# Optimization experiments

Measured on AMD Instinct MI355X. Metric: run time of the kernel, lower is better.

Reference implementation:

```python
import jax, jax.numpy as jnp
import numpy as np
import math

EPS = 1e-6  # PCEN eps


def _logit(p):
    return math.log(p / (1.0 - p))


def _pcen(mel, log_s, log_alpha, log_delta, log_r, dmin, dmax):
    """PCEN: per-channel energy normalization. mel: (B, M, T); params: (M,)."""
    s = jnp.clip(jax.nn.sigmoid(log_s), 0.05, 0.3)            # (M,)
    alpha = jnp.clip(jax.nn.sigmoid(log_alpha), 0.9, 0.999)   # (M,)
    delta = jnp.clip(jnp.exp(log_delta), dmin, dmax)          # (M,)
    r = jnp.clip(jax.nn.sigmoid(log_r), 0.05, 0.25)           # (M,)

    # IIR smoother over time: smoother_0 = mel[..., 0];
    # for t in 0..T-1: smoother = (1-s)*smoother + s*mel_t  (t=0 included -> smoothed_0 = mel_0)
    mel_t = jnp.transpose(mel, (2, 0, 1))  # (T, B, M)

    def step(sm, x):
        sm = (1.0 - s) * sm + s * x
        return sm, sm

    _, smoothed_t = jax.lax.scan(step, mel_t[0], mel_t)
    smoothed = jnp.transpose(smoothed_t, (1, 2, 0))  # (B, M, T)

    gain = (EPS + smoothed) ** (-alpha[None, :, None])
    d = delta[None, :, None]
    rr = r[None, :, None]
    return (mel * gain + d) ** rr - d ** rr


def setup_inputs() -> dict:
    key = jax.random.key(0)
    B, M, T = 64, 80, 4000
    mel = jax.random.uniform(key, (B, M, T), dtype=jnp.float32)
    f = jnp.full
    return {
        "mel": mel,
        # non-stationary expert PCEN (s=0.025, alpha=0.99, delta=2.0, r=0.5)
        "log_s_ns": f((M,), _logit(0.025), jnp.float32),
        "log_alpha_ns": f((M,), _logit(0.99), jnp.float32),
        "log_delta_ns": f((M,), math.log(2.0), jnp.float32),
        "log_r_ns": f((M,), _logit(0.5), jnp.float32),
        # stationary expert PCEN (s=0.15, alpha=0.99, delta=0.01, r=0.1)
        "log_s_st": f((M,), _logit(0.15), jnp.float32),
        "log_alpha_st": f((M,), _logit(0.99), jnp.float32),
        "log_delta_st": f((M,), math.log(0.01), jnp.float32),
        "log_r_st": f((M,), _logit(0.1), jnp.float32),
        "gate_temp": jnp.asarray(5.0, jnp.float32),
    }


def reference(mel, log_s_ns, log_alpha_ns, log_delta_ns, log_r_ns,
              log_s_st, log_alpha_st, log_delta_st, log_r_st, gate_temp):
    out_ns = _pcen(mel, log_s_ns, log_alpha_ns, log_delta_ns, log_r_ns, 0.5, 5.0)
    out_st = _pcen(mel, log_s_st, log_alpha_st, log_delta_st, log_r_st, 0.001, 0.1)

    # routing signal: spectral flatness + spectral tilt (0 learnable params)
    log_mel = jnp.log(mel + 1e-8)
    geo = jnp.exp(jnp.mean(log_mel, axis=1, keepdims=True))          # (B,1,T)
    arith = jnp.mean(mel, axis=1, keepdims=True) + 1e-8
    sf = jnp.clip(geo / arith, 0.0, 1.0)

    M = mel.shape[1]
    low = jnp.mean(mel[:, : M // 3, :], axis=1, keepdims=True)
    high = jnp.mean(mel[:, 2 * M // 3 :, :], axis=1, keepdims=True)
    tilt = jnp.clip(low / (low + high + 1e-8), 0.0, 1.0)

    sf_adj = sf + (1.0 - sf) * jax.nn.relu(tilt - 0.6)
    gate = jax.nn.sigmoid(gate_temp * (sf_adj - 0.5))
    return gate * out_st + (1.0 - gate) * out_ns
```

## Files before the change

kernel.cpp:

```cpp
#include <hip/hip_runtime.h>
#include <math.h>

static constexpr int kM = 80;
static constexpr int kT = 4000;
static constexpr int kB = 64;
static constexpr int kLow = kM / 3;
static constexpr int kHighStart = 2 * kM / 3;
static constexpr int kHighCount = kM - kHighStart;
#define EPSF 1e-6f
#define LOG2E 1.4426950408889634f

typedef float vfloat4 __attribute__((ext_vector_type(4)));

__device__ __forceinline__ float hw_exp2(float x) { return __builtin_amdgcn_exp2f(x); }
__device__ __forceinline__ float hw_log2(float x) { return __builtin_amdgcn_logf(x); }

__device__ __forceinline__ float fast_sigmoid(float x) {
    return __builtin_amdgcn_rcpf(1.0f + hw_exp2(-x * LOG2E));
}

__global__ __launch_bounds__(256) void gate_kernel(
    const float* __restrict__ mel,
    const float* __restrict__ gate_temp,
    float* __restrict__ gate)
{
    const int lane = threadIdx.x & 63;
    const int wid  = threadIdx.x >> 6;
    const int b    = blockIdx.y;
    const int t0   = blockIdx.x * 256 + lane * 4;
    const bool valid = (t0 < kT);

    const float* base = mel + (size_t)b * kM * kT + t0;

    vfloat4 slog = {0.f,0.f,0.f,0.f}, ssum = {0.f,0.f,0.f,0.f};
    vfloat4 slow = {0.f,0.f,0.f,0.f}, shigh = {0.f,0.f,0.f,0.f};

    const int m0 = wid * 20;
    if (valid) {
        #pragma unroll
        for (int j = 0; j < 20; ++j) {
            const int m = m0 + j;
            const vfloat4 v = *reinterpret_cast<const vfloat4*>(base + (size_t)m * kT);
            vfloat4 lg;
            lg.x = hw_log2(v.x + 1e-8f); lg.y = hw_log2(v.y + 1e-8f);
            lg.z = hw_log2(v.z + 1e-8f); lg.w = hw_log2(v.w + 1e-8f);
            slog += lg;
            ssum += v;
            if (m < kLow)       slow  += v;
            if (m >= kHighStart) shigh += v;
        }
    }

    __shared__ vfloat4 sh[4][4][64];
    sh[wid][0][lane] = slog;
    sh[wid][1][lane] = ssum;
    sh[wid][2][lane] = slow;
    sh[wid][3][lane] = shigh;
    __syncthreads();

    if (wid == 0 && valid) {
        slog  = sh[0][0][lane] + sh[1][0][lane] + sh[2][0][lane] + sh[3][0][lane];
        ssum  = sh[0][1][lane] + sh[1][1][lane] + sh[2][1][lane] + sh[3][1][lane];
        slow  = sh[0][2][lane] + sh[1][2][lane] + sh[2][2][lane] + sh[3][2][lane];
        shigh = sh[0][3][lane] + sh[1][3][lane] + sh[2][3][lane] + sh[3][3][lane];

        const float gt = gate_temp[0];
        float sl[4]  = {slog.x, slog.y, slog.z, slog.w};
        float ss[4]  = {ssum.x, ssum.y, ssum.z, ssum.w};
        float lo[4]  = {slow.x, slow.y, slow.z, slow.w};
        float hi[4]  = {shigh.x, shigh.y, shigh.z, shigh.w};
        float g4[4];
        #pragma unroll
        for (int q = 0; q < 4; ++q) {
            const float geo   = hw_exp2(sl[q] * (1.0f / kM));
            const float arith = ss[q] * (1.0f / kM) + 1e-8f;
            float sf = geo * __builtin_amdgcn_rcpf(arith);
            sf = fminf(fmaxf(sf, 0.0f), 1.0f);
            const float low  = lo[q] * (1.0f / kLow);
            const float high = hi[q] * (1.0f / kHighCount);
            float tilt = low * __builtin_amdgcn_rcpf(low + high + 1e-8f);
            tilt = fminf(fmaxf(tilt, 0.0f), 1.0f);
            const float sfa = sf + (1.0f - sf) * fmaxf(tilt - 0.6f, 0.0f);
            g4[q] = fast_sigmoid(gt * (sfa - 0.5f));
        }
        vfloat4 o; o.x = g4[0]; o.y = g4[1]; o.z = g4[2]; o.w = g4[3];
        *reinterpret_cast<vfloat4*>(gate + (size_t)b * kT + t0) = o;
    }
}

__global__ __launch_bounds__(256) void pcen_kernel(
    const float* __restrict__ mel,
    const float* __restrict__ ls_ns, const float* __restrict__ la_ns,
    const float* __restrict__ ld_ns, const float* __restrict__ lr_ns,
    const float* __restrict__ ls_st, const float* __restrict__ la_st,
    const float* __restrict__ ld_st, const float* __restrict__ lr_st,
    const float* __restrict__ gate,
    float* __restrict__ out)
{
    const int m = blockIdx.x;
    const int b = blockIdx.y;

    const float s_ns     = fminf(fmaxf(fast_sigmoid(ls_ns[m]), 0.05f), 0.3f);
    const float alpha_ns = fminf(fmaxf(fast_sigmoid(la_ns[m]), 0.9f), 0.999f);
    const float delta_ns = fminf(fmaxf(hw_exp2(ld_ns[m] * LOG2E), 0.5f), 5.0f);
    const float r_ns     = fminf(fmaxf(fast_sigmoid(lr_ns[m]), 0.05f), 0.25f);
    const float s_st     = fminf(fmaxf(fast_sigmoid(ls_st[m]), 0.05f), 0.3f);
    const float alpha_st = fminf(fmaxf(fast_sigmoid(la_st[m]), 0.9f), 0.999f);
    const float delta_st = fminf(fmaxf(hw_exp2(ld_st[m] * LOG2E), 0.001f), 0.1f);
    const float r_st     = fminf(fmaxf(fast_sigmoid(lr_st[m]), 0.05f), 0.25f);
    const float dr_ns = hw_exp2(r_ns * hw_log2(delta_ns));
    const float dr_st = hw_exp2(r_st * hw_log2(delta_st));
    const float a_ns = 1.0f - s_ns;
    const float a_st = 1.0f - s_st;
    const float man = -alpha_ns, mas = -alpha_st;

    const size_t rowoff = ((size_t)b * kM + m) * kT;
    const float* row = mel + rowoff;

    const int tid = threadIdx.x;
    const int t0  = tid * 16;
    const bool valid = (t0 < kT);

    float x[16];
    if (valid) {
        const float4* p = reinterpret_cast<const float4*>(row + t0);
        #pragma unroll
        for (int q = 0; q < 4; ++q) {
            const float4 v = p[q];
            x[4*q+0] = v.x; x[4*q+1] = v.y; x[4*q+2] = v.z; x[4*q+3] = v.w;
        }
    } else {
        #pragma unroll
        for (int k = 0; k < 16; ++k) x[k] = 0.0f;
    }

    __shared__ float sv0;
    if (tid == 0) sv0 = x[0];

    float An = 1.0f, Bn = 0.0f, As = 1.0f, Bs = 0.0f;
    if (valid) {
        #pragma unroll
        for (int k = 0; k < 16; ++k) {
            Bn = fmaf(a_ns, Bn, s_ns * x[k]);
            Bs = fmaf(a_st, Bs, s_st * x[k]);
        }
        const float a2n = a_ns*a_ns, a4n = a2n*a2n, a8n = a4n*a4n;
        const float a2s = a_st*a_st, a4s = a2s*a2s, a8s = a4s*a4s;
        An = a8n * a8n;
        As = a8s * a8s;
    }

    const int lane = tid & 63;
    const int wid  = tid >> 6;

    #pragma unroll
    for (int d = 1; d < 64; d <<= 1) {
        const float qAn = __shfl_up(An, d);
        const float qBn = __shfl_up(Bn, d);
        const float qAs = __shfl_up(As, d);
        const float qBs = __shfl_up(Bs, d);
        if (lane >= d) {
            Bn = fmaf(An, qBn, Bn); An = An * qAn;
            Bs = fmaf(As, qBs, Bs); As = As * qAs;
        }
    }

    __shared__ float wAn[4], wBn[4], wAs[4], wBs[4];
    if (lane == 63) { wAn[wid] = An; wBn[wid] = Bn; wAs[wid] = As; wBs[wid] = Bs; }
    __syncthreads();

    float eAn = __shfl_up(An, 1);
    float eBn = __shfl_up(Bn, 1);
    float eAs = __shfl_up(As, 1);
    float eBs = __shfl_up(Bs, 1);
    if (lane == 0) { eAn = 1.0f; eBn = 0.0f; eAs = 1.0f; eBs = 0.0f; }

    float pAn = 1.0f, pBn = 0.0f, pAs = 1.0f, pBs = 0.0f;
    for (int j = 0; j < wid; ++j) {
        pBn = fmaf(wAn[j], pBn, wBn[j]); pAn = wAn[j] * pAn;
        pBs = fmaf(wAs[j], pBs, wBs[j]); pAs = wAs[j] * pAs;
    }

    const float v0 = sv0;
    float smn = fmaf(eAn, fmaf(pAn, v0, pBn), eBn);
    float sms = fmaf(eAs, fmaf(pAs, v0, pBs), eBs);

    if (valid) {
        float gv[16];
        const float4* gp = reinterpret_cast<const float4*>(gate + (size_t)b * kT + t0);
        #pragma unroll
        for (int q = 0; q < 4; ++q) {
            const float4 v = gp[q];
            gv[4*q+0] = v.x; gv[4*q+1] = v.y; gv[4*q+2] = v.z; gv[4*q+3] = v.w;
        }

        float res[16];
        #pragma unroll
        for (int k = 0; k < 16; ++k) {
            const float xv = x[k];
            smn = fmaf(a_ns, smn, s_ns * xv);
            sms = fmaf(a_st, sms, s_st * xv);
            const float un = fmaf(xv, hw_exp2(man * hw_log2(smn + EPSF)), delta_ns);
            const float on = hw_exp2(r_ns * hw_log2(un)) - dr_ns;
            const float us = fmaf(xv, hw_exp2(mas * hw_log2(sms + EPSF)), delta_st);
            const float os = hw_exp2(r_st * hw_log2(us)) - dr_st;
            res[k] = fmaf(gv[k], os - on, on);
        }

        float4* op = reinterpret_cast<float4*>(out + rowoff + t0);
        #pragma unroll
        for (int q = 0; q < 4; ++q) {
            float4 v;
            v.x = res[4*q+0]; v.y = res[4*q+1]; v.z = res[4*q+2]; v.w = res[4*q+3];
            op[q] = v;
        }
    }
}

extern "C" void kernel_launch(void* const* d_in, const int* in_sizes, int n_in,
                              void* d_out, int out_size, void* d_ws, size_t ws_size,
                              hipStream_t stream)
{
    const float* mel       = (const float*)d_in[0];
    const float* ls_ns     = (const float*)d_in[1];
    const float* la_ns     = (const float*)d_in[2];
    const float* ld_ns     = (const float*)d_in[3];
    const float* lr_ns     = (const float*)d_in[4];
    const float* ls_st     = (const float*)d_in[5];
    const float* la_st     = (const float*)d_in[6];
    const float* ld_st     = (const float*)d_in[7];
    const float* lr_st     = (const float*)d_in[8];
    const float* gate_temp = (const float*)d_in[9];
    float* out  = (float*)d_out;
    float* gate = (float*)d_ws;

    dim3 gA(16, kB);
    gate_kernel<<<gA, 256, 0, stream>>>(mel, gate_temp, gate);

    dim3 gB(kM, kB);
    pcen_kernel<<<gB, 256, 0, stream>>>(mel, ls_ns, la_ns, ld_ns, lr_ns,
                                        ls_st, la_st, ld_st, lr_st, gate, out);
}
```

Before: 184.5 us.

## Split batch into two phases for L2 reuse and pack dual PCEN math into float2

The launch now runs the gate and PCEN kernels over two batch halves in sequence, instead of one gate pass over the whole batch followed by one PCEN pass. The aim is to keep each half of mel (about 41 MB) resident in cache between the gate reduction and the PCEN pass, so PCEN rereads hit cache rather than HBM. The two PCEN branches' scan and elementwise arithmetic are also packed into float2 vectors so the compiler can emit packed FP32 instructions. The cost is two extra kernel launches and smaller grids per phase, which may leave less parallelism to hide the serial scan.

```diff
diff --git a/kernel.cpp b/kernel.cpp
--- a/kernel.cpp
+++ b/kernel.cpp
@@ -7,10 +7,13 @@
 static constexpr int kLow = kM / 3;
 static constexpr int kHighStart = 2 * kM / 3;
 static constexpr int kHighCount = kM - kHighStart;
+static constexpr int kPhases = 2;
+static constexpr int kBPhase = kB / kPhases;
 #define EPSF 1e-6f
 #define LOG2E 1.4426950408889634f
 
 typedef float vfloat4 __attribute__((ext_vector_type(4)));
+typedef float vfloat2 __attribute__((ext_vector_type(2)));
 
 __device__ __forceinline__ float hw_exp2(float x) { return __builtin_amdgcn_exp2f(x); }
 __device__ __forceinline__ float hw_log2(float x) { return __builtin_amdgcn_logf(x); }
@@ -22,11 +25,12 @@
 __global__ __launch_bounds__(256) void gate_kernel(
     const float* __restrict__ mel,
     const float* __restrict__ gate_temp,
-    float* __restrict__ gate)
+    float* __restrict__ gate,
+    int b0)
 {
     const int lane = threadIdx.x & 63;
     const int wid  = threadIdx.x >> 6;
-    const int b    = blockIdx.y;
+    const int b    = b0 + blockIdx.y;
     const int t0   = blockIdx.x * 256 + lane * 4;
     const bool valid = (t0 < kT);
 
@@ -46,7 +50,7 @@
             lg.z = hw_log2(v.z + 1e-8f); lg.w = hw_log2(v.w + 1e-8f);
             slog += lg;
             ssum += v;
-            if (m < kLow)       slow  += v;
+            if (m < kLow)        slow  += v;
             if (m >= kHighStart) shigh += v;
         }
     }
@@ -95,10 +99,11 @@
     const float* __restrict__ ls_st, const float* __restrict__ la_st,
     const float* __restrict__ ld_st, const float* __restrict__ lr_st,
     const float* __restrict__ gate,
-    float* __restrict__ out)
+    float* __restrict__ out,
+    int b0)
 {
     const int m = blockIdx.x;
-    const int b = blockIdx.y;
+    const int b = b0 + blockIdx.y;
 
     const float s_ns     = fminf(fmaxf(fast_sigmoid(ls_ns[m]), 0.05f), 0.3f);
     const float alpha_ns = fminf(fmaxf(fast_sigmoid(la_ns[m]), 0.9f), 0.999f);
@@ -110,8 +115,10 @@
     const float r_st     = fminf(fmaxf(fast_sigmoid(lr_st[m]), 0.05f), 0.25f);
     const float dr_ns = hw_exp2(r_ns * hw_log2(delta_ns));
     const float dr_st = hw_exp2(r_st * hw_log2(delta_st));
-    const float a_ns = 1.0f - s_ns;
-    const float a_st = 1.0f - s_st;
+
+    const vfloat2 a2 = {1.0f - s_ns, 1.0f - s_st};
+    const vfloat2 s2 = {s_ns, s_st};
+    const vfloat2 d2 = {delta_ns, delta_st};
     const float man = -alpha_ns, mas = -alpha_st;
 
     const size_t rowoff = ((size_t)b * kM + m) * kT;
@@ -137,17 +144,16 @@
     __shared__ float sv0;
     if (tid == 0) sv0 = x[0];
 
-    float An = 1.0f, Bn = 0.0f, As = 1.0f, Bs = 0.0f;
+    vfloat2 Av = {1.0f, 1.0f}, Bv = {0.0f, 0.0f};
     if (valid) {
         #pragma unroll
         for (int k = 0; k < 16; ++k) {
-            Bn = fmaf(a_ns, Bn, s_ns * x[k]);
-            Bs = fmaf(a_st, Bs, s_st * x[k]);
-        }
-        const float a2n = a_ns*a_ns, a4n = a2n*a2n, a8n = a4n*a4n;
-        const float a2s = a_st*a_st, a4s = a2s*a2s, a8s = a4s*a4s;
-        An = a8n * a8n;
-        As = a8s * a8s;
+            Bv = a2 * Bv + s2 * x[k];
+        }
+        const vfloat2 p2 = a2 * a2;
+        const vfloat2 p4 = p2 * p2;
+        const vfloat2 p8 = p4 * p4;
+        Av = p8 * p8;
     }
 
     const int lane = tid & 63;
@@ -155,35 +161,35 @@
 
     #pragma unroll
     for (int d = 1; d < 64; d <<= 1) {
-        const float qAn = __shfl_up(An, d);
-        const float qBn = __shfl_up(Bn, d);
-        const float qAs = __shfl_up(As, d);
-        const float qBs = __shfl_up(Bs, d);
+        const float qAn = __shfl_up(Av.x, d);
+        const float qAs = __shfl_up(Av.y, d);
+        const float qBn = __shfl_up(Bv.x, d);
+        const float qBs = __shfl_up(Bv.y, d);
         if (lane >= d) {
-            Bn = fmaf(An, qBn, Bn); An = An * qAn;
-            Bs = fmaf(As, qBs, Bs); As = As * qAs;
-        }
-    }
-
-    __shared__ float wAn[4], wBn[4], wAs[4], wBs[4];
-    if (lane == 63) { wAn[wid] = An; wBn[wid] = Bn; wAs[wid] = As; wBs[wid] = Bs; }
+            const vfloat2 qA = {qAn, qAs};
+            const vfloat2 qB = {qBn, qBs};
+            Bv = Av * qB + Bv;
+            Av = Av * qA;
+        }
+    }
+
+    __shared__ vfloat2 wA[4], wB[4];
+    if (lane == 63) { wA[wid] = Av; wB[wid] = Bv; }
     __syncthreads();
 
-    float eAn = __shfl_up(An, 1);
-    float eBn = __shfl_up(Bn, 1);
-    float eAs = __shfl_up(As, 1);
-    float eBs = __shfl_up(Bs, 1);
-    if (lane == 0) { eAn = 1.0f; eBn = 0.0f; eAs = 1.0f; eBs = 0.0f; }
-
-    float pAn = 1.0f, pBn = 0.0f, pAs = 1.0f, pBs = 0.0f;
+    vfloat2 eA, eB;
+    eA.x = __shfl_up(Av.x, 1); eA.y = __shfl_up(Av.y, 1);
+    eB.x = __shfl_up(Bv.x, 1); eB.y = __shfl_up(Bv.y, 1);
+    if (lane == 0) { eA = (vfloat2){1.0f, 1.0f}; eB = (vfloat2){0.0f, 0.0f}; }
+
+    vfloat2 pA = {1.0f, 1.0f}, pB = {0.0f, 0.0f};
     for (int j = 0; j < wid; ++j) {
-        pBn = fmaf(wAn[j], pBn, wBn[j]); pAn = wAn[j] * pAn;
-        pBs = fmaf(wAs[j], pBs, wBs[j]); pAs = wAs[j] * pAs;
-    }
-
-    const float v0 = sv0;
-    float smn = fmaf(eAn, fmaf(pAn, v0, pBn), eBn);
-    float sms = fmaf(eAs, fmaf(pAs, v0, pBs), eBs);
+        pB = wA[j] * pB + wB[j];
+        pA = wA[j] * pA;
+    }
+
+    const vfloat2 v0 = {sv0, sv0};
+    vfloat2 sm = eA * (pA * v0 + pB) + eB;
 
     if (valid) {
         float gv[16];
@@ -198,12 +204,13 @@
         #pragma unroll
         for (int k = 0; k < 16; ++k) {
             const float xv = x[k];
-            smn = fmaf(a_ns, smn, s_ns * xv);
-            sms = fmaf(a_st, sms, s_st * xv);
-            const float un = fmaf(xv, hw_exp2(man * hw_log2(smn + EPSF)), delta_ns);
-            const float on = hw_exp2(r_ns * hw_log2(un)) - dr_ns;
-            const float us = fmaf(xv, hw_exp2(mas * hw_log2(sms + EPSF)), delta_st);
-            const float os = hw_exp2(r_st * hw_log2(us)) - dr_st;
+            sm = a2 * sm + s2 * xv;
+            vfloat2 g2;
+            g2.x = hw_exp2(man * hw_log2(sm.x + EPSF));
+            g2.y = hw_exp2(mas * hw_log2(sm.y + EPSF));
+            const vfloat2 u2 = g2 * xv + d2;
+            const float on = hw_exp2(r_ns * hw_log2(u2.x)) - dr_ns;
+            const float os = hw_exp2(r_st * hw_log2(u2.y)) - dr_st;
             res[k] = fmaf(gv[k], os - on, on);
         }
 
@@ -234,10 +241,12 @@
     float* out  = (float*)d_out;
     float* gate = (float*)d_ws;
 
-    dim3 gA(16, kB);
-    gate_kernel<<<gA, 256, 0, stream>>>(mel, gate_temp, gate);
-
-    dim3 gB(kM, kB);
-    pcen_kernel<<<gB, 256, 0, stream>>>(mel, ls_ns, la_ns, ld_ns, lr_ns,
-                                        ls_st, la_st, ld_st, lr_st, gate, out);
-}
+    for (int p = 0; p < kPhases; ++p) {
+        const int b0 = p * kBPhase;
+        dim3 gA(16, kBPhase);
+        gate_kernel<<<gA, 256, 0, stream>>>(mel, gate_temp, gate, b0);
+        dim3 gB(kM, kBPhase);
+        pcen_kernel<<<gB, 256, 0, stream>>>(mel, ls_ns, la_ns, ld_ns, lr_ns,
+                                            ls_st, la_st, ld_st, lr_st, gate, out, b0);
+    }
+}
```

New measurement: 193.8 us. 5.1% more time.
